# Kernel optimization log

Hardware: AMD Instinct MI355X
Metric: run time of the kernel (lower is better)

Reference implementation:

```python
import jax, jax.numpy as jnp
import numpy as np

DIM = 1024
HEADS = 16
DIM_HEAD = 64
INNER = HEADS * DIM_HEAD
SCALE = DIM_HEAD ** -0.5
LN_EPS = 1e-5
MASK_VALUE = -np.finfo(np.float32).max


def setup_inputs() -> dict:
    key = jax.random.key(0)
    ks = jax.random.split(key, 3)
    x = jax.random.normal(ks[0], (2, 2048, DIM), dtype=jnp.float32)
    w_qkv = jax.random.normal(ks[1], (DIM, 3 * INNER), dtype=jnp.float32) * (DIM ** -0.5)
    w_out = jax.random.normal(ks[2], (INNER, DIM), dtype=jnp.float32) * (INNER ** -0.5)
    ln_gamma = jnp.ones((DIM,), dtype=jnp.float32)
    ln_beta = jnp.zeros((DIM,), dtype=jnp.float32)
    return {"x": x, "ln_gamma": ln_gamma, "ln_beta": ln_beta, "w_qkv": w_qkv, "w_out": w_out}


def reference(x, ln_gamma, ln_beta, w_qkv, w_out):
    b, n, _ = x.shape
    # LayerNorm
    mu = jnp.mean(x, axis=-1, keepdims=True)
    var = jnp.mean(jnp.square(x - mu), axis=-1, keepdims=True)
    xn = (x - mu) * jax.lax.rsqrt(var + LN_EPS) * ln_gamma + ln_beta
    # QKV projection, split into heads: b n (h d) -> b h n d
    qkv = xn @ w_qkv  # [b, n, 3*inner]
    q, k, v = jnp.split(qkv, 3, axis=-1)
    def to_heads(t):
        return t.reshape(b, n, HEADS, DIM_HEAD).transpose(0, 2, 1, 3)
    q, k, v = to_heads(q), to_heads(k), to_heads(v)
    # scaled scores with diagonal excluded
    dots = jnp.einsum('bhnd,bhmd->bhnm', q, k) * SCALE
    eye = jnp.eye(n, dtype=bool)
    dots = jnp.where(eye, MASK_VALUE, dots)
    attn = jax.nn.softmax(dots, axis=-1)
    out = jnp.einsum('bhnm,bhmd->bhnd', attn, v)
    out = out.transpose(0, 2, 1, 3).reshape(b, n, INNER)
    return out @ w_out
```

## Files before the change

kernel.cpp:

```cpp
#include <hip/hip_runtime.h>


#define DIMM   1024
#define NSEQ   2048
#define BATCH  2
#define HEADS  16
#define DHEAD  64
#define QKVN   3072
#define MROWS  4096

typedef float          f32x4  __attribute__((ext_vector_type(4)));
typedef __bf16         bf16x8 __attribute__((ext_vector_type(8)));
typedef __bf16         bf16x4 __attribute__((ext_vector_type(4)));
typedef unsigned short u16x8  __attribute__((ext_vector_type(8)));
typedef unsigned short u16x4  __attribute__((ext_vector_type(4)));

#define QSCALE (0.125f * 1.4426950408889634f)

#if __has_builtin(__builtin_amdgcn_exp2f)
#define EXP2(x) __builtin_amdgcn_exp2f(x)
#else
#define EXP2(x) exp2f(x)
#endif

__device__ __forceinline__ unsigned short f2bf(float f) {
  unsigned u = __builtin_bit_cast(unsigned, f);
  u += 0x7FFFu + ((u >> 16) & 1u);
  return (unsigned short)(u >> 16);
}
__device__ __forceinline__ bf16x8 as_bf(u16x8 v) { return __builtin_bit_cast(bf16x8, v); }

__device__ __forceinline__ u16x4 cvt4(f32x4 v) {
  bf16x4 b;
  b[0] = (__bf16)v[0]; b[1] = (__bf16)v[1]; b[2] = (__bf16)v[2]; b[3] = (__bf16)v[3];
  return __builtin_bit_cast(u16x4, b);
}

__device__ __forceinline__ void gl_lds16(const unsigned short* g, unsigned short* l) {
  __builtin_amdgcn_global_load_lds(
      (const __attribute__((address_space(1))) unsigned*)g,
      (__attribute__((address_space(3))) unsigned*)l, 16, 0, 0);
}

__device__ __forceinline__ bf16x8 lds_frag(const unsigned short* base, int row, int chunk) {
  return as_bf(*(const u16x8*)&base[row * 64 + ((chunk ^ (row & 7)) << 3)]);
}

__device__ __forceinline__ void transpose_tile(
    const float* __restrict__ src, unsigned short* __restrict__ dst,
    int R, int C, int bx, int by, int tid) {
  __shared__ float t[32][33];
  const int rb = by * 32, cb = bx * 32;
  const int r0 = tid >> 5;
  const int c  = tid & 31;
#pragma unroll
  for (int i = 0; i < 4; ++i)
    t[r0 + i * 8][c] = src[(rb + r0 + i * 8) * C + cb + c];
  __syncthreads();
#pragma unroll
  for (int i = 0; i < 4; ++i)
    dst[(cb + r0 + i * 8) * R + rb + c] = f2bf(t[c][r0 + i * 8]);
}

__global__ __launch_bounds__(256) void prep_kernel(
    const float* __restrict__ x, const float* __restrict__ g,
    const float* __restrict__ be, const float* __restrict__ w_qkv,
    const float* __restrict__ w_out, unsigned short* __restrict__ xn,
    unsigned short* __restrict__ wqkvT, unsigned short* __restrict__ woutT) {
  const int bid = blockIdx.x, tid = threadIdx.x;
  if (bid < MROWS) {
    const int row = bid;
    const int wave = tid >> 6, lane = tid & 63;
    const float4 v = *(const float4*)&x[row * DIMM + tid * 4];
    float s  = v.x + v.y + v.z + v.w;
    float s2 = v.x * v.x + v.y * v.y + v.z * v.z + v.w * v.w;
#pragma unroll
    for (int o = 32; o >= 1; o >>= 1) { s += __shfl_xor(s, o); s2 += __shfl_xor(s2, o); }
    __shared__ float ps[4], ps2[4];
    if (lane == 0) { ps[wave] = s; ps2[wave] = s2; }
    __syncthreads();
    s  = ps[0] + ps[1] + ps[2] + ps[3];
    s2 = ps2[0] + ps2[1] + ps2[2] + ps2[3];
    const float mu  = s * (1.0f / DIMM);
    const float var = s2 * (1.0f / DIMM) - mu * mu;
    const float rs  = rsqrtf(var + 1e-5f);
    const float4 gg = *(const float4*)&g[tid * 4];
    const float4 bb = *(const float4*)&be[tid * 4];
    u16x4 o;
    o[0] = f2bf((v.x - mu) * rs * gg.x + bb.x);
    o[1] = f2bf((v.y - mu) * rs * gg.y + bb.y);
    o[2] = f2bf((v.z - mu) * rs * gg.z + bb.z);
    o[3] = f2bf((v.w - mu) * rs * gg.w + bb.w);
    *(u16x4*)&xn[row * DIMM + tid * 4] = o;
  } else {
    const int t = bid - MROWS;
    const int bx = t & 127, by = t >> 7;
    if (bx < QKVN / 32) transpose_tile(w_qkv, wqkvT, DIMM, QKVN, bx, by, tid);
    else                transpose_tile(w_out, woutT, DIMM, DIMM, bx - QKVN / 32, by, tid);
  }
}

__global__ __launch_bounds__(256, 2) void gemm_qkv_kernel(
    const unsigned short* __restrict__ A, const unsigned short* __restrict__ Bt,
    unsigned short* __restrict__ qb, unsigned short* __restrict__ kb,
    unsigned short* __restrict__ vtb) {
  __shared__ __attribute__((aligned(16))) unsigned short As[2 * 128 * 64];
  __shared__ __attribute__((aligned(16))) unsigned short Bs[2 * 128 * 64];
  const int tid = threadIdx.x;
  const int bm = blockIdx.y, bn = blockIdx.x;
  const int lane = tid & 63, wave = tid >> 6;
  const int l15 = lane & 15, quad = lane >> 4;
  const int wm = wave >> 1, wn = wave & 1;
  const int lrow = lane >> 3;
  const int gcol = ((lane & 7) ^ lrow) << 3;
  const unsigned short* Ab = A  + (bm * 128 + wave * 32 + lrow) * DIMM + gcol;
  const unsigned short* Bb = Bt + (bn * 128 + wave * 32 + lrow) * DIMM + gcol;
  const bool swap = (bn < 16);
  f32x4 acc[4][4] = {};

#pragma unroll
  for (int j = 0; j < 4; ++j) {
    gl_lds16(Ab + j * 8 * DIMM, &As[(wave * 32 + j * 8) * 64]);
    gl_lds16(Bb + j * 8 * DIMM, &Bs[(wave * 32 + j * 8) * 64]);
  }
  for (int it = 0; it < DIMM / 64; ++it) {
    const int cur = it & 1;
    __syncthreads();
    if (it < DIMM / 64 - 1) {
      const int k0 = (it + 1) * 64;
      unsigned short* An = &As[(cur ^ 1) * 8192];
      unsigned short* Bn = &Bs[(cur ^ 1) * 8192];
#pragma unroll
      for (int j = 0; j < 4; ++j) {
        gl_lds16(Ab + j * 8 * DIMM + k0, &An[(wave * 32 + j * 8) * 64]);
        gl_lds16(Bb + j * 8 * DIMM + k0, &Bn[(wave * 32 + j * 8) * 64]);
      }
    }
    const unsigned short* Ac = &As[cur * 8192];
    const unsigned short* Bc = &Bs[cur * 8192];
#pragma unroll
    for (int kk = 0; kk < 2; ++kk) {
      bf16x8 af[4], bfr[4];
#pragma unroll
      for (int mi = 0; mi < 4; ++mi) af[mi]  = lds_frag(Ac, wm * 64 + mi * 16 + l15, kk * 4 + quad);
#pragma unroll
      for (int ni = 0; ni < 4; ++ni) bfr[ni] = lds_frag(Bc, wn * 64 + ni * 16 + l15, kk * 4 + quad);
      if (swap) {
#pragma unroll
        for (int mi = 0; mi < 4; ++mi)
#pragma unroll
          for (int ni = 0; ni < 4; ++ni)
            acc[mi][ni] = __builtin_amdgcn_mfma_f32_16x16x32_bf16(bfr[ni], af[mi], acc[mi][ni], 0, 0, 0);
      } else {
#pragma unroll
        for (int mi = 0; mi < 4; ++mi)
#pragma unroll
          for (int ni = 0; ni < 4; ++ni)
            acc[mi][ni] = __builtin_amdgcn_mfma_f32_16x16x32_bf16(af[mi], bfr[ni], acc[mi][ni], 0, 0, 0);
      }
    }
  }

  if (swap) {
    const int colbase = bn * 128 + wn * 64;
    const int which = colbase >> 10;
    unsigned short* dst = which ? kb : qb;
    const float sc = which ? 1.0f : QSCALE;
#pragma unroll
    for (int mi = 0; mi < 4; ++mi) {
      const int m = bm * 128 + wm * 64 + mi * 16 + l15;
      const int bh0 = (m >> 11) * HEADS;
      const int n = m & 2047;
#pragma unroll
      for (int ni = 0; ni < 4; ++ni) {
        const int wc = (colbase & 1023) + ni * 16 + quad * 4;
        const int h = wc >> 6, dd = wc & 63;
        f32x4 v = acc[mi][ni] * sc;
        *(u16x4*)&dst[((bh0 + h) * NSEQ + n) * DHEAD + dd] = cvt4(v);
      }
    }
  } else {
    const int colbase = bn * 128 + wn * 64 - 2048;
#pragma unroll
    for (int mi = 0; mi < 4; ++mi) {
      const int m0 = bm * 128 + wm * 64 + mi * 16 + quad * 4;
      const int bh0 = (m0 >> 11) * HEADS;
      const int n0 = m0 & 2047;
#pragma unroll
      for (int ni = 0; ni < 4; ++ni) {
        const int vcol = colbase + ni * 16 + l15;
        const int h = vcol >> 6, dd = vcol & 63;
        *(u16x4*)&vtb[((bh0 + h) * DHEAD + dd) * NSEQ + n0] = cvt4(acc[mi][ni]);
      }
    }
  }
}

__global__ __launch_bounds__(256, 2) void attn_kernel(
    const unsigned short* __restrict__ qb, const unsigned short* __restrict__ kb,
    const unsigned short* __restrict__ vtb, unsigned short* __restrict__ attn_out) {
  __shared__ __attribute__((aligned(16))) unsigned short Ks[2][64 * 64];
  __shared__ __attribute__((aligned(16))) unsigned short Vts[2][64 * 64];
  __shared__ __attribute__((aligned(16))) unsigned short Ps[4][2][16][72];
  const int tid = threadIdx.x, wave = tid >> 6, lane = tid & 63;
  const int l15 = lane & 15, quad = lane >> 4;
  const int bh = blockIdx.x, qt = blockIdx.y;
  const int b = bh >> 4, h = bh & 15;
  const int qbase = qt * 128 + wave * 32;

  bf16x8 aq[2][2];
#pragma unroll
  for (int sub = 0; sub < 2; ++sub) {
    const unsigned short* qrow = qb + (bh * NSEQ + qbase + sub * 16 + l15) * DHEAD;
    aq[sub][0] = as_bf(*(const u16x8*)(qrow + quad * 8));
    aq[sub][1] = as_bf(*(const u16x8*)(qrow + 32 + quad * 8));
  }

  float lsum[2] = {0.f, 0.f};
  f32x4 occ[2][4] = {};

  const int lrow = lane >> 3;
  const int gcol = ((lane & 7) ^ lrow) << 3;
  const unsigned short* Kb = kb  + (bh * NSEQ + wave * 16 + lrow) * DHEAD + gcol;
  const unsigned short* Vb = vtb + (bh * DHEAD + wave * 16 + lrow) * NSEQ + gcol;

  gl_lds16(Kb,             &Ks[0][(wave * 16) * 64]);
  gl_lds16(Kb + 8 * DHEAD, &Ks[0][(wave * 16 + 8) * 64]);
  gl_lds16(Vb,             &Vts[0][(wave * 16) * 64]);
  gl_lds16(Vb + 8 * NSEQ,  &Vts[0][(wave * 16 + 8) * 64]);

  const int diag_it = qt * 2 + (wave >> 1);

  for (int it = 0; it < NSEQ / 64; ++it) {
    const int cur = it & 1;
    __syncthreads();
    if (it < NSEQ / 64 - 1) {
      const unsigned short* Kn = Kb + (it + 1) * 64 * DHEAD;
      const unsigned short* Vn = Vb + (it + 1) * 64;
      gl_lds16(Kn,             &Ks[cur ^ 1][(wave * 16) * 64]);
      gl_lds16(Kn + 8 * DHEAD, &Ks[cur ^ 1][(wave * 16 + 8) * 64]);
      gl_lds16(Vn,             &Vts[cur ^ 1][(wave * 16) * 64]);
      gl_lds16(Vn + 8 * NSEQ,  &Vts[cur ^ 1][(wave * 16 + 8) * 64]);
    }
    bf16x8 ak[2][4], av[2][4];
#pragma unroll
    for (int kk = 0; kk < 2; ++kk)
#pragma unroll
      for (int ct = 0; ct < 4; ++ct) {
        ak[kk][ct] = lds_frag(&Ks[cur][0],  ct * 16 + l15, kk * 4 + quad);
        av[kk][ct] = lds_frag(&Vts[cur][0], ct * 16 + l15, kk * 4 + quad);
      }
#pragma unroll
    for (int sub = 0; sub < 2; ++sub) {
      f32x4 scc[4];
#pragma unroll
      for (int ct = 0; ct < 4; ++ct) scc[ct] = (f32x4){-32.f, -32.f, -32.f, -32.f};
#pragma unroll
      for (int kk = 0; kk < 2; ++kk)
#pragma unroll
        for (int ct = 0; ct < 4; ++ct)
          scc[ct] = __builtin_amdgcn_mfma_f32_16x16x32_bf16(ak[kk][ct], aq[sub][kk], scc[ct], 0, 0, 0);
#pragma unroll
      for (int ct = 0; ct < 4; ++ct)
#pragma unroll
        for (int r = 0; r < 4; ++r) scc[ct][r] = EXP2(scc[ct][r]);

      if (it == diag_it) {
        const int kvo_want = (wave & 1) * 32 + sub * 16 + l15;
#pragma unroll
        for (int ct = 0; ct < 4; ++ct)
#pragma unroll
          for (int r = 0; r < 4; ++r)
            if (ct * 16 + quad * 4 + r == kvo_want) scc[ct][r] = 0.f;
      }

      f32x4 ps4 = (scc[0] + scc[1]) + (scc[2] + scc[3]);
      lsum[sub] += (ps4[0] + ps4[1]) + (ps4[2] + ps4[3]);

#pragma unroll
      for (int ct = 0; ct < 4; ++ct)
        *(u16x4*)&Ps[wave][sub][l15][ct * 16 + quad * 4] = cvt4(scc[ct]);

#pragma unroll
      for (int kk = 0; kk < 2; ++kk) {
        bf16x8 bp = as_bf(*(const u16x8*)&Ps[wave][sub][l15][kk * 32 + quad * 8]);
#pragma unroll
        for (int ct = 0; ct < 4; ++ct)
          occ[sub][ct] = __builtin_amdgcn_mfma_f32_16x16x32_bf16(av[kk][ct], bp, occ[sub][ct], 0, 0, 0);
      }
    }
  }
#pragma unroll
  for (int sub = 0; sub < 2; ++sub) {
    float l = lsum[sub];
    l += __shfl_xor(l, 16);
    l += __shfl_xor(l, 32);
    const float rl = __builtin_amdgcn_rcpf(l);
    const int qg = qbase + sub * 16 + l15;
#pragma unroll
    for (int ct = 0; ct < 4; ++ct) {
      f32x4 ov = occ[sub][ct] * rl;
      *(u16x4*)&attn_out[(b * NSEQ + qg) * DIMM + h * DHEAD + ct * 16 + quad * 4] = cvt4(ov);
    }
  }
}

__global__ __launch_bounds__(256, 2) void gemm_out_kernel(
    const unsigned short* __restrict__ A,
    const unsigned short* __restrict__ Bt,
    float* __restrict__ out) {
  __shared__ __attribute__((aligned(16))) unsigned short As[2 * 64 * 64];
  __shared__ __attribute__((aligned(16))) unsigned short Bs[2 * 128 * 64];
  const int tid = threadIdx.x;
  const int bm = blockIdx.y, bn = blockIdx.x;
  const int lane = tid & 63, wave = tid >> 6;
  const int l15 = lane & 15, quad = lane >> 4;
  const int wm = wave >> 1, wn = wave & 1;
  const int lrow = lane >> 3;
  const int gcol = ((lane & 7) ^ lrow) << 3;
  const unsigned short* Ab = A  + (bm * 64 + wave * 16 + lrow) * DIMM + gcol;
  const unsigned short* Bb = Bt + (bn * 128 + wave * 32 + lrow) * DIMM + gcol;
  f32x4 acc[2][4] = {};

#pragma unroll
  for (int j = 0; j < 2; ++j) gl_lds16(Ab + j * 8 * DIMM, &As[(wave * 16 + j * 8) * 64]);
#pragma unroll
  for (int j = 0; j < 4; ++j) gl_lds16(Bb + j * 8 * DIMM, &Bs[(wave * 32 + j * 8) * 64]);

  for (int it = 0; it < DIMM / 64; ++it) {
    const int cur = it & 1;
    __syncthreads();
    if (it < DIMM / 64 - 1) {
      const int k0 = (it + 1) * 64;
      unsigned short* An = &As[(cur ^ 1) * 4096];
      unsigned short* Bn = &Bs[(cur ^ 1) * 8192];
#pragma unroll
      for (int j = 0; j < 2; ++j) gl_lds16(Ab + j * 8 * DIMM + k0, &An[(wave * 16 + j * 8) * 64]);
#pragma unroll
      for (int j = 0; j < 4; ++j) gl_lds16(Bb + j * 8 * DIMM + k0, &Bn[(wave * 32 + j * 8) * 64]);
    }
    const unsigned short* Ac = &As[cur * 4096];
    const unsigned short* Bc = &Bs[cur * 8192];
#pragma unroll
    for (int kk = 0; kk < 2; ++kk) {
      bf16x8 af[2], bfr[4];
#pragma unroll
      for (int mi = 0; mi < 2; ++mi) af[mi]  = lds_frag(Ac, wm * 32 + mi * 16 + l15, kk * 4 + quad);
#pragma unroll
      for (int ni = 0; ni < 4; ++ni) bfr[ni] = lds_frag(Bc, wn * 64 + ni * 16 + l15, kk * 4 + quad);
#pragma unroll
      for (int mi = 0; mi < 2; ++mi)
#pragma unroll
        for (int ni = 0; ni < 4; ++ni)
          acc[mi][ni] = __builtin_amdgcn_mfma_f32_16x16x32_bf16(bfr[ni], af[mi], acc[mi][ni], 0, 0, 0);
    }
  }
#pragma unroll
  for (int mi = 0; mi < 2; ++mi) {
    const int m = bm * 64 + wm * 32 + mi * 16 + l15;
#pragma unroll
    for (int ni = 0; ni < 4; ++ni) {
      const int col = bn * 128 + wn * 64 + ni * 16 + quad * 4;
      *(f32x4*)&out[m * DIMM + col] = acc[mi][ni];
    }
  }
}

extern "C" void kernel_launch(void* const* d_in, const int* in_sizes, int n_in,
                              void* d_out, int out_size, void* d_ws, size_t ws_size,
                              hipStream_t stream) {
  const float* x     = (const float*)d_in[0];
  const float* gamma = (const float*)d_in[1];
  const float* beta  = (const float*)d_in[2];
  const float* w_qkv = (const float*)d_in[3];
  const float* w_out = (const float*)d_in[4];
  float* out = (float*)d_out;

  char* ws = (char*)d_ws;
  unsigned short* xn    = (unsigned short*)(ws);
  unsigned short* wqkvT = (unsigned short*)(ws + 8388608);
  unsigned short* woutT = (unsigned short*)(ws + 14680064);
  unsigned short* qbuf  = (unsigned short*)(ws + 16777216);
  unsigned short* kbuf  = (unsigned short*)(ws + 25165824);
  unsigned short* vtbuf = (unsigned short*)(ws + 33554432);
  unsigned short* attnb = (unsigned short*)(ws + 41943040);

  prep_kernel<<<MROWS + (QKVN + DIMM) / 32 * (DIMM / 32), 256, 0, stream>>>(
      x, gamma, beta, w_qkv, w_out, xn, wqkvT, woutT);
  gemm_qkv_kernel<<<dim3(24, MROWS / 128), 256, 0, stream>>>(xn, wqkvT, qbuf, kbuf, vtbuf);
  attn_kernel<<<dim3(BATCH * HEADS, NSEQ / 128), 256, 0, stream>>>(qbuf, kbuf, vtbuf, attnb);
  gemm_out_kernel<<<dim3(DIMM / 128, MROWS / 64), 256, 0, stream>>>(attnb, woutT, out);
}
```

Before: 188.1 us.

## Single-buffer QKV GEMM and split attention into 8 waves per block

The QKV GEMM drops its double-buffered LDS tiles for a single buffer with load/sync/compute/sync steps, halving shared memory so three blocks can share a CU. The attention kernel doubles the block to 512 threads so each wave owns 16 query rows instead of 32, which cuts accumulator registers and raises occupancy. The cost is losing the load/compute overlap in the GEMM and fewer MFMAs per K/V fragment load in attention, so each LDS fragment read feeds less work.

Result: no change. 189.8 us (+0.9%).

```diff
diff --git a/kernel.cpp b/kernel.cpp
--- a/kernel.cpp
+++ b/kernel.cpp
@@ -100,12 +100,12 @@
   }
 }
 
-__global__ __launch_bounds__(256, 2) void gemm_qkv_kernel(
+__global__ __launch_bounds__(256, 3) void gemm_qkv_kernel(
     const unsigned short* __restrict__ A, const unsigned short* __restrict__ Bt,
     unsigned short* __restrict__ qb, unsigned short* __restrict__ kb,
     unsigned short* __restrict__ vtb) {
-  __shared__ __attribute__((aligned(16))) unsigned short As[2 * 128 * 64];
-  __shared__ __attribute__((aligned(16))) unsigned short Bs[2 * 128 * 64];
+  __shared__ __attribute__((aligned(16))) unsigned short As[128 * 64];
+  __shared__ __attribute__((aligned(16))) unsigned short Bs[128 * 64];
   const int tid = threadIdx.x;
   const int bm = blockIdx.y, bn = blockIdx.x;
   const int lane = tid & 63, wave = tid >> 6;
@@ -118,33 +118,20 @@
   const bool swap = (bn < 16);
   f32x4 acc[4][4] = {};
 
-#pragma unroll
-  for (int j = 0; j < 4; ++j) {
-    gl_lds16(Ab + j * 8 * DIMM, &As[(wave * 32 + j * 8) * 64]);
-    gl_lds16(Bb + j * 8 * DIMM, &Bs[(wave * 32 + j * 8) * 64]);
-  }
-  for (int it = 0; it < DIMM / 64; ++it) {
-    const int cur = it & 1;
-    __syncthreads();
-    if (it < DIMM / 64 - 1) {
-      const int k0 = (it + 1) * 64;
-      unsigned short* An = &As[(cur ^ 1) * 8192];
-      unsigned short* Bn = &Bs[(cur ^ 1) * 8192];
-#pragma unroll
-      for (int j = 0; j < 4; ++j) {
-        gl_lds16(Ab + j * 8 * DIMM + k0, &An[(wave * 32 + j * 8) * 64]);
-        gl_lds16(Bb + j * 8 * DIMM + k0, &Bn[(wave * 32 + j * 8) * 64]);
-      }
-    }
-    const unsigned short* Ac = &As[cur * 8192];
-    const unsigned short* Bc = &Bs[cur * 8192];
+  for (int k0 = 0; k0 < DIMM; k0 += 64) {
+#pragma unroll
+    for (int j = 0; j < 4; ++j) {
+      gl_lds16(Ab + j * 8 * DIMM + k0, &As[(wave * 32 + j * 8) * 64]);
+      gl_lds16(Bb + j * 8 * DIMM + k0, &Bs[(wave * 32 + j * 8) * 64]);
+    }
+    __syncthreads();
 #pragma unroll
     for (int kk = 0; kk < 2; ++kk) {
       bf16x8 af[4], bfr[4];
 #pragma unroll
-      for (int mi = 0; mi < 4; ++mi) af[mi]  = lds_frag(Ac, wm * 64 + mi * 16 + l15, kk * 4 + quad);
-#pragma unroll
-      for (int ni = 0; ni < 4; ++ni) bfr[ni] = lds_frag(Bc, wn * 64 + ni * 16 + l15, kk * 4 + quad);
+      for (int mi = 0; mi < 4; ++mi) af[mi]  = lds_frag(As, wm * 64 + mi * 16 + l15, kk * 4 + quad);
+#pragma unroll
+      for (int ni = 0; ni < 4; ++ni) bfr[ni] = lds_frag(Bs, wn * 64 + ni * 16 + l15, kk * 4 + quad);
       if (swap) {
 #pragma unroll
         for (int mi = 0; mi < 4; ++mi)
@@ -159,6 +146,7 @@
             acc[mi][ni] = __builtin_amdgcn_mfma_f32_16x16x32_bf16(af[mi], bfr[ni], acc[mi][ni], 0, 0, 0);
       }
     }
+    __syncthreads();
   }
 
   if (swap) {
@@ -196,51 +184,45 @@
   }
 }
 
-__global__ __launch_bounds__(256, 2) void attn_kernel(
+__global__ __launch_bounds__(512, 4) void attn_kernel(
     const unsigned short* __restrict__ qb, const unsigned short* __restrict__ kb,
     const unsigned short* __restrict__ vtb, unsigned short* __restrict__ attn_out) {
   __shared__ __attribute__((aligned(16))) unsigned short Ks[2][64 * 64];
   __shared__ __attribute__((aligned(16))) unsigned short Vts[2][64 * 64];
-  __shared__ __attribute__((aligned(16))) unsigned short Ps[4][2][16][72];
+  __shared__ __attribute__((aligned(16))) unsigned short Ps[8][16][72];
   const int tid = threadIdx.x, wave = tid >> 6, lane = tid & 63;
   const int l15 = lane & 15, quad = lane >> 4;
   const int bh = blockIdx.x, qt = blockIdx.y;
   const int b = bh >> 4, h = bh & 15;
-  const int qbase = qt * 128 + wave * 32;
-
-  bf16x8 aq[2][2];
-#pragma unroll
-  for (int sub = 0; sub < 2; ++sub) {
-    const unsigned short* qrow = qb + (bh * NSEQ + qbase + sub * 16 + l15) * DHEAD;
-    aq[sub][0] = as_bf(*(const u16x8*)(qrow + quad * 8));
-    aq[sub][1] = as_bf(*(const u16x8*)(qrow + 32 + quad * 8));
-  }
-
-  float lsum[2] = {0.f, 0.f};
-  f32x4 occ[2][4] = {};
+  const int qg = qt * 128 + wave * 16 + l15;
+
+  bf16x8 aq[2];
+  {
+    const unsigned short* qrow = qb + (bh * NSEQ + qg) * DHEAD;
+    aq[0] = as_bf(*(const u16x8*)(qrow + quad * 8));
+    aq[1] = as_bf(*(const u16x8*)(qrow + 32 + quad * 8));
+  }
+
+  float lsum = 0.f;
+  f32x4 occ[4] = {};
 
   const int lrow = lane >> 3;
   const int gcol = ((lane & 7) ^ lrow) << 3;
-  const unsigned short* Kb = kb  + (bh * NSEQ + wave * 16 + lrow) * DHEAD + gcol;
-  const unsigned short* Vb = vtb + (bh * DHEAD + wave * 16 + lrow) * NSEQ + gcol;
-
-  gl_lds16(Kb,             &Ks[0][(wave * 16) * 64]);
-  gl_lds16(Kb + 8 * DHEAD, &Ks[0][(wave * 16 + 8) * 64]);
-  gl_lds16(Vb,             &Vts[0][(wave * 16) * 64]);
-  gl_lds16(Vb + 8 * NSEQ,  &Vts[0][(wave * 16 + 8) * 64]);
-
-  const int diag_it = qt * 2 + (wave >> 1);
+  const unsigned short* Kb = kb  + (bh * NSEQ + wave * 8 + lrow) * DHEAD + gcol;
+  const unsigned short* Vb = vtb + (bh * DHEAD + wave * 8 + lrow) * NSEQ + gcol;
+
+  gl_lds16(Kb, &Ks[0][(wave * 8) * 64]);
+  gl_lds16(Vb, &Vts[0][(wave * 8) * 64]);
+
+  const int diag_it = qt * 2 + (wave >> 2);
+  const int kvo_want = (wave & 3) * 16 + l15;
 
   for (int it = 0; it < NSEQ / 64; ++it) {
     const int cur = it & 1;
     __syncthreads();
     if (it < NSEQ / 64 - 1) {
-      const unsigned short* Kn = Kb + (it + 1) * 64 * DHEAD;
-      const unsigned short* Vn = Vb + (it + 1) * 64;
-      gl_lds16(Kn,             &Ks[cur ^ 1][(wave * 16) * 64]);
-      gl_lds16(Kn + 8 * DHEAD, &Ks[cur ^ 1][(wave * 16 + 8) * 64]);
-      gl_lds16(Vn,             &Vts[cur ^ 1][(wave * 16) * 64]);
-      gl_lds16(Vn + 8 * NSEQ,  &Vts[cur ^ 1][(wave * 16 + 8) * 64]);
+      gl_lds16(Kb + (it + 1) * 64 * DHEAD, &Ks[cur ^ 1][(wave * 8) * 64]);
+      gl_lds16(Vb + (it + 1) * 64,         &Vts[cur ^ 1][(wave * 8) * 64]);
     }
     bf16x8 ak[2][4], av[2][4];
 #pragma unroll
@@ -250,58 +232,49 @@
         ak[kk][ct] = lds_frag(&Ks[cur][0],  ct * 16 + l15, kk * 4 + quad);
         av[kk][ct] = lds_frag(&Vts[cur][0], ct * 16 + l15, kk * 4 + quad);
       }
-#pragma unroll
-    for (int sub = 0; sub < 2; ++sub) {
-      f32x4 scc[4];
-#pragma unroll
-      for (int ct = 0; ct < 4; ++ct) scc[ct] = (f32x4){-32.f, -32.f, -32.f, -32.f};
-#pragma unroll
-      for (int kk = 0; kk < 2; ++kk)
-#pragma unroll
-        for (int ct = 0; ct < 4; ++ct)
-          scc[ct] = __builtin_amdgcn_mfma_f32_16x16x32_bf16(ak[kk][ct], aq[sub][kk], scc[ct], 0, 0, 0);
+    f32x4 scc[4];
+#pragma unroll
+    for (int ct = 0; ct < 4; ++ct) scc[ct] = (f32x4){-32.f, -32.f, -32.f, -32.f};
+#pragma unroll
+    for (int kk = 0; kk < 2; ++kk)
 #pragma unroll
       for (int ct = 0; ct < 4; ++ct)
-#pragma unroll
-        for (int r = 0; r < 4; ++r) scc[ct][r] = EXP2(scc[ct][r]);
-
-      if (it == diag_it) {
-        const int kvo_want = (wave & 1) * 32 + sub * 16 + l15;
-#pragma unroll
-        for (int ct = 0; ct < 4; ++ct)
-#pragma unroll
-          for (int r = 0; r < 4; ++r)
-            if (ct * 16 + quad * 4 + r == kvo_want) scc[ct][r] = 0.f;
-      }
-
-      f32x4 ps4 = (scc[0] + scc[1]) + (scc[2] + scc[3]);
-      lsum[sub] += (ps4[0] + ps4[1]) + (ps4[2] + ps4[3]);
-
+        scc[ct] = __builtin_amdgcn_mfma_f32_16x16x32_bf16(ak[kk][ct], aq[kk], scc[ct], 0, 0, 0);
+#pragma unroll
+    for (int ct = 0; ct < 4; ++ct)
+#pragma unroll
+      for (int r = 0; r < 4; ++r) scc[ct][r] = EXP2(scc[ct][r]);
+
+    if (it == diag_it) {
 #pragma unroll
       for (int ct = 0; ct < 4; ++ct)
-        *(u16x4*)&Ps[wave][sub][l15][ct * 16 + quad * 4] = cvt4(scc[ct]);
-
-#pragma unroll
-      for (int kk = 0; kk < 2; ++kk) {
-        bf16x8 bp = as_bf(*(const u16x8*)&Ps[wave][sub][l15][kk * 32 + quad * 8]);
-#pragma unroll
-        for (int ct = 0; ct < 4; ++ct)
-          occ[sub][ct] = __builtin_amdgcn_mfma_f32_16x16x32_bf16(av[kk][ct], bp, occ[sub][ct], 0, 0, 0);
-      }
-    }
-  }
-#pragma unroll
-  for (int sub = 0; sub < 2; ++sub) {
-    float l = lsum[sub];
-    l += __shfl_xor(l, 16);
-    l += __shfl_xor(l, 32);
-    const float rl = __builtin_amdgcn_rcpf(l);
-    const int qg = qbase + sub * 16 + l15;
-#pragma unroll
-    for (int ct = 0; ct < 4; ++ct) {
-      f32x4 ov = occ[sub][ct] * rl;
-      *(u16x4*)&attn_out[(b * NSEQ + qg) * DIMM + h * DHEAD + ct * 16 + quad * 4] = cvt4(ov);
-    }
+#pragma unroll
+        for (int r = 0; r < 4; ++r)
+          if (ct * 16 + quad * 4 + r == kvo_want) scc[ct][r] = 0.f;
+    }
+
+    f32x4 ps4 = (scc[0] + scc[1]) + (scc[2] + scc[3]);
+    lsum += (ps4[0] + ps4[1]) + (ps4[2] + ps4[3]);
+
+#pragma unroll
+    for (int ct = 0; ct < 4; ++ct)
+      *(u16x4*)&Ps[wave][l15][ct * 16 + quad * 4] = cvt4(scc[ct]);
+
+#pragma unroll
+    for (int kk = 0; kk < 2; ++kk) {
+      bf16x8 bp = as_bf(*(const u16x8*)&Ps[wave][l15][kk * 32 + quad * 8]);
+#pragma unroll
+      for (int ct = 0; ct < 4; ++ct)
+        occ[ct] = __builtin_amdgcn_mfma_f32_16x16x32_bf16(av[kk][ct], bp, occ[ct], 0, 0, 0);
+    }
+  }
+  lsum += __shfl_xor(lsum, 16);
+  lsum += __shfl_xor(lsum, 32);
+  const float rl = __builtin_amdgcn_rcpf(lsum);
+#pragma unroll
+  for (int ct = 0; ct < 4; ++ct) {
+    f32x4 ov = occ[ct] * rl;
+    *(u16x4*)&attn_out[(b * NSEQ + qg) * DIMM + h * DHEAD + ct * 16 + quad * 4] = cvt4(ov);
   }
 }
 
@@ -388,6 +361,6 @@
   prep_kernel<<<MROWS + (QKVN + DIMM) / 32 * (DIMM / 32), 256, 0, stream>>>(
       x, gamma, beta, w_qkv, w_out, xn, wqkvT, woutT);
   gemm_qkv_kernel<<<dim3(24, MROWS / 128), 256, 0, stream>>>(xn, wqkvT, qbuf, kbuf, vtbuf);
-  attn_kernel<<<dim3(BATCH * HEADS, NSEQ / 128), 256, 0, stream>>>(qbuf, kbuf, vtbuf, attnb);
+  attn_kernel<<<dim3(BATCH * HEADS, NSEQ / 128), 512, 0, stream>>>(qbuf, kbuf, vtbuf, attnb);
   gemm_out_kernel<<<dim3(DIMM / 128, MROWS / 64), 256, 0, stream>>>(attnb, woutT, out);
 }
```

## Drop LDS double buffering in GEMMs for occupancy; widen out-GEMM K tile

Applied to the files above, without the earlier changes.

The QKV GEMM swaps its double-buffered LDS prefetch for a single buffer with load, sync, compute, sync, and raises launch bounds to three blocks per CU so more waves can hide latency. The output GEMM also goes single-buffered and widens the K step from 64 to 128, using a new 128-wide swizzled LDS layout, which halves the number of loop iterations and barriers. The cost is that global-to-LDS loads no longer overlap with MFMA work inside a block, so throughput now depends on other resident blocks covering that latency.

New measurement: 183.1 us. 1.03x faster.

```diff
diff --git a/kernel.cpp b/kernel.cpp
--- a/kernel.cpp
+++ b/kernel.cpp
@@ -44,6 +44,10 @@
 
 __device__ __forceinline__ bf16x8 lds_frag(const unsigned short* base, int row, int chunk) {
   return as_bf(*(const u16x8*)&base[row * 64 + ((chunk ^ (row & 7)) << 3)]);
+}
+
+__device__ __forceinline__ bf16x8 lds_frag128(const unsigned short* base, int row, int chunk) {
+  return as_bf(*(const u16x8*)&base[row * 128 + ((chunk ^ (row & 15)) << 3)]);
 }
 
 __device__ __forceinline__ void transpose_tile(
@@ -100,12 +104,12 @@
   }
 }
 
-__global__ __launch_bounds__(256, 2) void gemm_qkv_kernel(
+__global__ __launch_bounds__(256, 3) void gemm_qkv_kernel(
     const unsigned short* __restrict__ A, const unsigned short* __restrict__ Bt,
     unsigned short* __restrict__ qb, unsigned short* __restrict__ kb,
     unsigned short* __restrict__ vtb) {
-  __shared__ __attribute__((aligned(16))) unsigned short As[2 * 128 * 64];
-  __shared__ __attribute__((aligned(16))) unsigned short Bs[2 * 128 * 64];
+  __shared__ __attribute__((aligned(16))) unsigned short As[128 * 64];
+  __shared__ __attribute__((aligned(16))) unsigned short Bs[128 * 64];
   const int tid = threadIdx.x;
   const int bm = blockIdx.y, bn = blockIdx.x;
   const int lane = tid & 63, wave = tid >> 6;
@@ -118,33 +122,20 @@
   const bool swap = (bn < 16);
   f32x4 acc[4][4] = {};
 
-#pragma unroll
-  for (int j = 0; j < 4; ++j) {
-    gl_lds16(Ab + j * 8 * DIMM, &As[(wave * 32 + j * 8) * 64]);
-    gl_lds16(Bb + j * 8 * DIMM, &Bs[(wave * 32 + j * 8) * 64]);
-  }
-  for (int it = 0; it < DIMM / 64; ++it) {
-    const int cur = it & 1;
-    __syncthreads();
-    if (it < DIMM / 64 - 1) {
-      const int k0 = (it + 1) * 64;
-      unsigned short* An = &As[(cur ^ 1) * 8192];
-      unsigned short* Bn = &Bs[(cur ^ 1) * 8192];
-#pragma unroll
-      for (int j = 0; j < 4; ++j) {
-        gl_lds16(Ab + j * 8 * DIMM + k0, &An[(wave * 32 + j * 8) * 64]);
-        gl_lds16(Bb + j * 8 * DIMM + k0, &Bn[(wave * 32 + j * 8) * 64]);
-      }
-    }
-    const unsigned short* Ac = &As[cur * 8192];
-    const unsigned short* Bc = &Bs[cur * 8192];
+  for (int k0 = 0; k0 < DIMM; k0 += 64) {
+#pragma unroll
+    for (int j = 0; j < 4; ++j) {
+      gl_lds16(Ab + j * 8 * DIMM + k0, &As[(wave * 32 + j * 8) * 64]);
+      gl_lds16(Bb + j * 8 * DIMM + k0, &Bs[(wave * 32 + j * 8) * 64]);
+    }
+    __syncthreads();
 #pragma unroll
     for (int kk = 0; kk < 2; ++kk) {
       bf16x8 af[4], bfr[4];
 #pragma unroll
-      for (int mi = 0; mi < 4; ++mi) af[mi]  = lds_frag(Ac, wm * 64 + mi * 16 + l15, kk * 4 + quad);
-#pragma unroll
-      for (int ni = 0; ni < 4; ++ni) bfr[ni] = lds_frag(Bc, wn * 64 + ni * 16 + l15, kk * 4 + quad);
+      for (int mi = 0; mi < 4; ++mi) af[mi]  = lds_frag(As, wm * 64 + mi * 16 + l15, kk * 4 + quad);
+#pragma unroll
+      for (int ni = 0; ni < 4; ++ni) bfr[ni] = lds_frag(Bs, wn * 64 + ni * 16 + l15, kk * 4 + quad);
       if (swap) {
 #pragma unroll
         for (int mi = 0; mi < 4; ++mi)
@@ -159,6 +150,7 @@
             acc[mi][ni] = __builtin_amdgcn_mfma_f32_16x16x32_bf16(af[mi], bfr[ni], acc[mi][ni], 0, 0, 0);
       }
     }
+    __syncthreads();
   }
 
   if (swap) {
@@ -309,51 +301,45 @@
     const unsigned short* __restrict__ A,
     const unsigned short* __restrict__ Bt,
     float* __restrict__ out) {
-  __shared__ __attribute__((aligned(16))) unsigned short As[2 * 64 * 64];
-  __shared__ __attribute__((aligned(16))) unsigned short Bs[2 * 128 * 64];
+  __shared__ __attribute__((aligned(16))) unsigned short As[64 * 128];
+  __shared__ __attribute__((aligned(16))) unsigned short Bs[128 * 128];
   const int tid = threadIdx.x;
   const int bm = blockIdx.y, bn = blockIdx.x;
   const int lane = tid & 63, wave = tid >> 6;
   const int l15 = lane & 15, quad = lane >> 4;
   const int wm = wave >> 1, wn = wave & 1;
-  const int lrow = lane >> 3;
-  const int gcol = ((lane & 7) ^ lrow) << 3;
-  const unsigned short* Ab = A  + (bm * 64 + wave * 16 + lrow) * DIMM + gcol;
-  const unsigned short* Bb = Bt + (bn * 128 + wave * 32 + lrow) * DIMM + gcol;
+  const int rl4 = lane >> 4;
+  const int cp  = lane & 15;
+  const int cx  = cp ^ rl4;
+  const int Arow0 = bm * 64 + wave * 16 + rl4;
+  const int Brow0 = bn * 128 + wave * 32 + rl4;
   f32x4 acc[2][4] = {};
 
-#pragma unroll
-  for (int j = 0; j < 2; ++j) gl_lds16(Ab + j * 8 * DIMM, &As[(wave * 16 + j * 8) * 64]);
-#pragma unroll
-  for (int j = 0; j < 4; ++j) gl_lds16(Bb + j * 8 * DIMM, &Bs[(wave * 32 + j * 8) * 64]);
-
-  for (int it = 0; it < DIMM / 64; ++it) {
-    const int cur = it & 1;
-    __syncthreads();
-    if (it < DIMM / 64 - 1) {
-      const int k0 = (it + 1) * 64;
-      unsigned short* An = &As[(cur ^ 1) * 4096];
-      unsigned short* Bn = &Bs[(cur ^ 1) * 8192];
-#pragma unroll
-      for (int j = 0; j < 2; ++j) gl_lds16(Ab + j * 8 * DIMM + k0, &An[(wave * 16 + j * 8) * 64]);
-#pragma unroll
-      for (int j = 0; j < 4; ++j) gl_lds16(Bb + j * 8 * DIMM + k0, &Bn[(wave * 32 + j * 8) * 64]);
-    }
-    const unsigned short* Ac = &As[cur * 4096];
-    const unsigned short* Bc = &Bs[cur * 8192];
-#pragma unroll
-    for (int kk = 0; kk < 2; ++kk) {
+  for (int it = 0; it < 8; ++it) {
+    const int k0 = it * 128;
+#pragma unroll
+    for (int j = 0; j < 4; ++j)
+      gl_lds16(A + (Arow0 + j * 4) * DIMM + k0 + ((cx ^ (j << 2)) << 3),
+               &As[(wave * 16 + j * 4) * 128]);
+#pragma unroll
+    for (int j = 0; j < 8; ++j)
+      gl_lds16(Bt + (Brow0 + j * 4) * DIMM + k0 + ((cx ^ ((j & 3) << 2)) << 3),
+               &Bs[(wave * 32 + j * 4) * 128]);
+    __syncthreads();
+#pragma unroll
+    for (int kk = 0; kk < 4; ++kk) {
       bf16x8 af[2], bfr[4];
 #pragma unroll
-      for (int mi = 0; mi < 2; ++mi) af[mi]  = lds_frag(Ac, wm * 32 + mi * 16 + l15, kk * 4 + quad);
-#pragma unroll
-      for (int ni = 0; ni < 4; ++ni) bfr[ni] = lds_frag(Bc, wn * 64 + ni * 16 + l15, kk * 4 + quad);
+      for (int mi = 0; mi < 2; ++mi) af[mi]  = lds_frag128(As, wm * 32 + mi * 16 + l15, kk * 4 + quad);
+#pragma unroll
+      for (int ni = 0; ni < 4; ++ni) bfr[ni] = lds_frag128(Bs, wn * 64 + ni * 16 + l15, kk * 4 + quad);
 #pragma unroll
       for (int mi = 0; mi < 2; ++mi)
 #pragma unroll
         for (int ni = 0; ni < 4; ++ni)
           acc[mi][ni] = __builtin_amdgcn_mfma_f32_16x16x32_bf16(bfr[ni], af[mi], acc[mi][ni], 0, 0, 0);
     }
+    __syncthreads();
   }
 #pragma unroll
   for (int mi = 0; mi < 2; ++mi) {
```
